# Kernel optimization log

Measured on AMD Instinct MI355X. Metric: run time of the kernel, lower is better.

The kernel has to match this reference:

```python
import jax, jax.numpy as jnp
import numpy as np

D_MODEL = 1024
H = 16
D_K = D_MODEL // H


def setup_inputs() -> dict:
    key = jax.random.key(0)
    ks = jax.random.split(key, 8)
    B, S = 2, 2048
    scale = 1.0 / np.sqrt(D_MODEL)
    return {
        "query": jax.random.normal(ks[0], (B, S, D_MODEL), dtype=jnp.float32),
        "key": jax.random.normal(ks[1], (B, S, D_MODEL), dtype=jnp.float32),
        "value": jax.random.normal(ks[2], (B, S, D_MODEL), dtype=jnp.float32),
        "mask": jnp.ones((B, 1, 1, S), dtype=jnp.int32),
        "Wq": jax.random.normal(ks[3], (D_MODEL, D_MODEL), dtype=jnp.float32) * scale,
        "Wk": jax.random.normal(ks[4], (D_MODEL, D_MODEL), dtype=jnp.float32) * scale,
        "Wv": jax.random.normal(ks[5], (D_MODEL, D_MODEL), dtype=jnp.float32) * scale,
        "Wo": jax.random.normal(ks[6], (D_MODEL, D_MODEL), dtype=jnp.float32) * scale,
    }


def reference(query, key, value, mask, Wq, Wk, Wv, Wo):
    # mask is a no-op in the original (masked_fill result discarded); dropout=0.
    B, S, _ = query.shape
    q = (query @ Wq.T).reshape(B, S, H, D_K)  # [B,S,H,Dk]
    k = (key @ Wk.T).reshape(B, S, H, D_K)
    v = (value @ Wv.T).reshape(B, S, H, D_K)
    # scores = Q K^T / sqrt(d_k)  -- NOTE: no softmax in the source module
    scores = jnp.einsum("bqhd,bkhd->bhqk", q, k) / jnp.sqrt(jnp.float32(D_K))
    out = jnp.einsum("bhqk,bkhd->bqhd", scores, v).reshape(B, S, D_MODEL)
    return out @ Wo.T
```

## Files before the change

### kernel.cpp

```cpp
#include <hip/hip_runtime.h>

#define DEV __device__ __forceinline__

typedef __attribute__((ext_vector_type(8))) short short8;
typedef __attribute__((ext_vector_type(4))) float f32x4;

DEV short f2bf(float x) {
  unsigned u = __float_as_uint(x);
  unsigned r = (u + 0x7fffu + ((u >> 16) & 1u)) >> 16;
  return (short)r;
}
DEV float bf2f(short x) {
  return __uint_as_float(((unsigned)(unsigned short)x) << 16);
}

DEV void gload_lds16(const void* g, void* l) {
  __builtin_amdgcn_global_load_lds((const __attribute__((address_space(1))) void*)g,
                                   (__attribute__((address_space(3))) void*)l, 16, 0, 0);
}

__global__ __launch_bounds__(256) void cvt_all(
    const float* __restrict__ s0, const float* __restrict__ s1,
    const float* __restrict__ s2, const float* __restrict__ s3,
    const float* __restrict__ s4, const float* __restrict__ s5,
    const float* __restrict__ s6,
    short* __restrict__ d0, short* __restrict__ d1, short* __restrict__ d2,
    short* __restrict__ d3, short* __restrict__ d4, short* __restrict__ d5,
    short* __restrict__ d6, float* __restrict__ Mb) {
  int g = blockIdx.x * 256 + threadIdx.x;
  if (g >= 2097152) {
    int off = g - 2097152;
    float4 z = {0.f, 0.f, 0.f, 0.f};
    float4* p = reinterpret_cast<float4*>(Mb) + (size_t)off * 2;
    p[0] = z;
    p[1] = z;
    return;
  }
  const float* s;
  short* d;
  int off;
  if (g < 524288) { s = s0; d = d0; off = g; }
  else if (g < 1048576) { s = s1; d = d1; off = g - 524288; }
  else if (g < 1572864) { s = s2; d = d2; off = g - 1048576; }
  else {
    int w2 = g - 1572864;
    int seg = w2 >> 17;
    off = w2 & 131071;
    s = seg == 0 ? s3 : seg == 1 ? s4 : seg == 2 ? s5 : s6;
    d = seg == 0 ? d3 : seg == 1 ? d4 : seg == 2 ? d5 : d6;
  }
  const float4* p = reinterpret_cast<const float4*>(s) + (size_t)off * 2;
  float4 a = p[0], b = p[1];
  short8 o;
  o[0] = f2bf(a.x); o[1] = f2bf(a.y); o[2] = f2bf(a.z); o[3] = f2bf(a.w);
  o[4] = f2bf(b.x); o[5] = f2bf(b.y); o[6] = f2bf(b.z); o[7] = f2bf(b.w);
  *reinterpret_cast<short8*>(d + (size_t)off * 8) = o;
}

template <typename OutT>
__global__ __launch_bounds__(256) void gemm_bt64(const short* __restrict__ A,
                                                 const short* __restrict__ W,
                                                 OutT* __restrict__ C,
                                                 long strideA, long strideW, long strideC) {
  __shared__ short At[128 * 64];
  __shared__ short Bt[64 * 64];
  const int nx = gridDim.x, ny = gridDim.y;
  int flat = blockIdx.x + nx * (blockIdx.y + ny * blockIdx.z);
  int nwg = nx * ny * gridDim.z;
  int l2 = (flat & 7) * (nwg >> 3) + (flat >> 3);
  int colB = l2 % nx;
  int tmp = l2 / nx;
  int rowB = tmp % ny;
  int zB = tmp / ny;

  const short* Ab = A + (size_t)zB * strideA;
  const short* Wb = W + (size_t)zB * strideW;
  OutT* Cb = C + (size_t)zB * strideC;
  const int t = threadIdx.x;
  const int w = t >> 6;
  const int l = t & 63;
  const int lg = l >> 4, lr = l & 15;
  const int wm = w >> 1, wn = w & 1;
  const int rowBase = rowB * 128;
  const int colBase = colB * 64;

  f32x4 acc[4][2] = {};

  for (int kt = 0; kt < 16; ++kt) {
    const int k0 = kt * 64;
    __syncthreads();
#pragma unroll
    for (int i = 0; i < 4; ++i) {
      int c = w * 256 + i * 64 + l;
      int r = c >> 3, s = c & 7;
      gload_lds16(Ab + (size_t)(rowBase + r) * 1024 + k0 + ((s ^ (r & 7)) << 3),
                  At + (size_t)c * 8);
    }
#pragma unroll
    for (int i = 0; i < 2; ++i) {
      int c = w * 128 + i * 64 + l;
      int r = c >> 3, s = c & 7;
      gload_lds16(Wb + (size_t)(colBase + r) * 1024 + k0 + ((s ^ (r & 7)) << 3),
                  Bt + (size_t)c * 8);
    }
    __syncthreads();
#pragma unroll
    for (int kk = 0; kk < 2; ++kk) {
      short8 bfr[2];
#pragma unroll
      for (int n = 0; n < 2; ++n) {
        int br = wn * 32 + n * 16 + lr;
        int slot = (kk * 4 + lg) ^ (br & 7);
        bfr[n] = *reinterpret_cast<const short8*>(&Bt[br * 64 + slot * 8]);
      }
#pragma unroll
      for (int m = 0; m < 4; ++m) {
        int ar = wm * 64 + m * 16 + lr;
        int slot = (kk * 4 + lg) ^ (ar & 7);
        short8 afr = *reinterpret_cast<const short8*>(&At[ar * 64 + slot * 8]);
        acc[m][0] = __builtin_amdgcn_mfma_f32_16x16x32_bf16(afr, bfr[0], acc[m][0], 0, 0, 0);
        acc[m][1] = __builtin_amdgcn_mfma_f32_16x16x32_bf16(afr, bfr[1], acc[m][1], 0, 0, 0);
      }
    }
  }
#pragma unroll
  for (int m = 0; m < 4; ++m)
#pragma unroll
    for (int n = 0; n < 2; ++n) {
      int row0 = rowBase + wm * 64 + m * 16 + lg * 4;
      int col = colBase + wn * 32 + n * 16 + lr;
#pragma unroll
      for (int j = 0; j < 4; ++j) {
        float v = acc[m][n][j];
        if constexpr (sizeof(OutT) == 2)
          Cb[(size_t)(row0 + j) * 1024 + col] = (OutT)f2bf(v);
        else
          Cb[(size_t)(row0 + j) * 1024 + col] = (OutT)v;
      }
    }
}

__global__ __launch_bounds__(256) void kv_outer(const short* __restrict__ Kp,
                                                const short* __restrict__ Vp,
                                                float* __restrict__ Mb) {
  __shared__ float Ks[128][64];
  __shared__ float Vs[128][64];
  const int t = threadIdx.x;
  const int sc = blockIdx.x, h = blockIdx.y, b = blockIdx.z;
  const size_t base = ((size_t)(b * 2048 + sc * 128)) * 1024 + h * 64;
  for (int e = t; e < 128 * 64; e += 256) {
    int r = e >> 6, c = e & 63;
    size_t g = base + (size_t)r * 1024 + c;
    Ks[r][c] = bf2f(Kp[g]);
    Vs[r][c] = bf2f(Vp[g]);
  }
  __syncthreads();
  const int dp0 = (t >> 4) * 4, d0 = (t & 15) * 4;
  float acc[4][4] = {};
  for (int s = 0; s < 128; ++s) {
    float4 kv = *reinterpret_cast<const float4*>(&Ks[s][dp0]);
    float4 vv = *reinterpret_cast<const float4*>(&Vs[s][d0]);
    float ka[4] = {kv.x, kv.y, kv.z, kv.w};
    float va[4] = {vv.x, vv.y, vv.z, vv.w};
#pragma unroll
    for (int i = 0; i < 4; ++i)
#pragma unroll
      for (int j = 0; j < 4; ++j) acc[i][j] += ka[i] * va[j];
  }
  float* dst = Mb + (size_t)(b * 16 + h) * 4096;
#pragma unroll
  for (int i = 0; i < 4; ++i)
#pragma unroll
    for (int j = 0; j < 4; ++j)
      atomicAdd(&dst[(dp0 + i) * 64 + d0 + j], acc[i][j] * 0.125f);
}

__global__ __launch_bounds__(256) void make_w2t(const float* __restrict__ Mb,
                                                const short* __restrict__ Wo,
                                                short* __restrict__ W2T) {
  __shared__ float Ms[64][65];
  __shared__ float Wos[64][64];
  const int t = threadIdx.x;
  const int jc = blockIdx.x, h = blockIdx.y, b = blockIdx.z;
  const float* Msrc = Mb + (size_t)(b * 16 + h) * 4096;
  for (int e = t; e < 4096; e += 256) {
    int r = e >> 6, c = e & 63;
    Ms[r][c] = Msrc[e];
    Wos[r][c] = bf2f(Wo[(size_t)(jc * 64 + r) * 1024 + h * 64 + c]);
  }
  __syncthreads();
  const int j0 = (t >> 4) * 4, p0 = (t & 15) * 4;
  float acc[4][4] = {};
  for (int d = 0; d < 64; ++d) {
    float wv[4], mv[4];
#pragma unroll
    for (int i = 0; i < 4; ++i) { wv[i] = Wos[j0 + i][d]; mv[i] = Ms[p0 + i][d]; }
#pragma unroll
    for (int i = 0; i < 4; ++i)
#pragma unroll
      for (int j2 = 0; j2 < 4; ++j2) acc[i][j2] += wv[i] * mv[j2];
  }
  short* dst = W2T + (size_t)b * 1048576;
#pragma unroll
  for (int i = 0; i < 4; ++i)
#pragma unroll
    for (int j2 = 0; j2 < 4; ++j2)
      dst[(size_t)(jc * 64 + j0 + i) * 1024 + h * 64 + p0 + j2] = f2bf(acc[i][j2]);
}

extern "C" void kernel_launch(void* const* d_in, const int* in_sizes, int n_in,
                              void* d_out, int out_size, void* d_ws, size_t ws_size,
                              hipStream_t stream) {
  const float* q  = (const float*)d_in[0];
  const float* k  = (const float*)d_in[1];
  const float* v  = (const float*)d_in[2];
  const float* Wq = (const float*)d_in[4];
  const float* Wk = (const float*)d_in[5];
  const float* Wv = (const float*)d_in[6];
  const float* Wo = (const float*)d_in[7];
  float* out = (float*)d_out;
  char* ws = (char*)d_ws;

  short* qkv = (short*)(ws);
  short* qb = qkv;
  short* kb = qkv + (size_t)4194304;
  short* vb = qkv + (size_t)8388608;
  short* wb = (short*)(ws + (24l << 20));
  short* wqb = wb;
  short* wkb = wb + 1048576;
  short* wvb = wb + 2097152;
  short* wob = wb + 3145728;
  short* Pp = (short*)(ws + (32l << 20));
  short* Qp = Pp;
  short* Kp = Pp + (size_t)4194304;
  short* Vp = Pp + (size_t)8388608;
  float* Mb  = (float*)(ws + (56l << 20));
  short* W2T = (short*)(ws + (57l << 20));

  cvt_all<<<8256, 256, 0, stream>>>(q, k, v, Wq, Wk, Wv, Wo,
                                    qb, kb, vb, wqb, wkb, wvb, wob, Mb);

  gemm_bt64<short><<<dim3(16, 32, 3), 256, 0, stream>>>(
      qkv, wb, Pp, 4194304l, 1048576l, 4194304l);

  kv_outer<<<dim3(16, 16, 2), 256, 0, stream>>>(Kp, Vp, Mb);

  make_w2t<<<dim3(16, 16, 2), 256, 0, stream>>>(Mb, wob, W2T);

  gemm_bt64<float><<<dim3(16, 16, 2), 256, 0, stream>>>(
      Qp, W2T, out, 2097152l, 1048576l, 2097152l);
}
```

Measured before the change: 209.1 us.

## Fuse fp32-to-bf16 conversion into QKV projection GEMM loads

Removes the separate conversion kernel and has the projection GEMM read fp32 inputs and weights directly, converting to bf16 in registers before writing swizzled LDS tiles. Global loads for the next k-tile are issued before the MFMA loop as register prefetch, and zeroing of the Mb accumulator moves into the first blocks. make_w2t now reads fp32 Wo directly. This drops a full kernel launch and the bf16 round trip through memory, but the GEMM reads twice as many bytes per tile, does its conversions inline, and no longer uses direct global-to-LDS loads.

```diff
diff --git a/kernel.cpp b/kernel.cpp
--- a/kernel.cpp
+++ b/kernel.cpp
@@ -19,42 +19,117 @@
                                    (__attribute__((address_space(3))) void*)l, 16, 0, 0);
 }
 
-__global__ __launch_bounds__(256) void cvt_all(
-    const float* __restrict__ s0, const float* __restrict__ s1,
-    const float* __restrict__ s2, const float* __restrict__ s3,
-    const float* __restrict__ s4, const float* __restrict__ s5,
-    const float* __restrict__ s6,
-    short* __restrict__ d0, short* __restrict__ d1, short* __restrict__ d2,
-    short* __restrict__ d3, short* __restrict__ d4, short* __restrict__ d5,
-    short* __restrict__ d6, float* __restrict__ Mb) {
-  int g = blockIdx.x * 256 + threadIdx.x;
-  if (g >= 2097152) {
-    int off = g - 2097152;
+__global__ __launch_bounds__(256) void gemm_proj_f32(
+    const float* __restrict__ q, const float* __restrict__ k, const float* __restrict__ v,
+    const float* __restrict__ Wq, const float* __restrict__ Wk, const float* __restrict__ Wv,
+    short* __restrict__ C, long strideC, float* __restrict__ Mb) {
+  __shared__ short At[128 * 64];
+  __shared__ short Bt[64 * 64];
+  const int t = threadIdx.x;
+  const int nx = gridDim.x, ny = gridDim.y;
+  int flat = blockIdx.x + nx * (blockIdx.y + ny * blockIdx.z);
+  int nwg = nx * ny * gridDim.z;
+  if (flat < 64) {
     float4 z = {0.f, 0.f, 0.f, 0.f};
-    float4* p = reinterpret_cast<float4*>(Mb) + (size_t)off * 2;
+    float4* p = reinterpret_cast<float4*>(Mb) + (size_t)flat * 512 + t * 2;
     p[0] = z;
     p[1] = z;
-    return;
-  }
-  const float* s;
-  short* d;
-  int off;
-  if (g < 524288) { s = s0; d = d0; off = g; }
-  else if (g < 1048576) { s = s1; d = d1; off = g - 524288; }
-  else if (g < 1572864) { s = s2; d = d2; off = g - 1048576; }
-  else {
-    int w2 = g - 1572864;
-    int seg = w2 >> 17;
-    off = w2 & 131071;
-    s = seg == 0 ? s3 : seg == 1 ? s4 : seg == 2 ? s5 : s6;
-    d = seg == 0 ? d3 : seg == 1 ? d4 : seg == 2 ? d5 : d6;
-  }
-  const float4* p = reinterpret_cast<const float4*>(s) + (size_t)off * 2;
-  float4 a = p[0], b = p[1];
-  short8 o;
-  o[0] = f2bf(a.x); o[1] = f2bf(a.y); o[2] = f2bf(a.z); o[3] = f2bf(a.w);
-  o[4] = f2bf(b.x); o[5] = f2bf(b.y); o[6] = f2bf(b.z); o[7] = f2bf(b.w);
-  *reinterpret_cast<short8*>(d + (size_t)off * 8) = o;
+  }
+  int l2 = (flat & 7) * (nwg >> 3) + (flat >> 3);
+  int colB = l2 % nx;
+  int tmp = l2 / nx;
+  int rowB = tmp % ny;
+  int zB = tmp / ny;
+
+  const float* Ab = zB == 0 ? q : zB == 1 ? k : v;
+  const float* Wb = zB == 0 ? Wq : zB == 1 ? Wk : Wv;
+  short* Cb = C + (size_t)zB * strideC;
+  const int w = t >> 6;
+  const int l = t & 63;
+  const int lg = l >> 4, lr = l & 15;
+  const int wm = w >> 1, wn = w & 1;
+  const int rowBase = rowB * 128;
+  const int colBase = colB * 64;
+
+  f32x4 acc[4][2] = {};
+  float4 ra[4][2], rw[2][2];
+
+#define LOAD_TILES(k0)                                                     \
+  {                                                                        \
+    _Pragma("unroll") for (int i = 0; i < 4; ++i) {                        \
+      int c = w * 256 + i * 64 + l;                                        \
+      int r = c >> 3, s = c & 7;                                           \
+      const float* src = Ab + (size_t)(rowBase + r) * 1024 + (k0) + s * 8; \
+      ra[i][0] = *reinterpret_cast<const float4*>(src);                    \
+      ra[i][1] = *reinterpret_cast<const float4*>(src + 4);                \
+    }                                                                      \
+    _Pragma("unroll") for (int i = 0; i < 2; ++i) {                        \
+      int c = w * 128 + i * 64 + l;                                        \
+      int r = c >> 3, s = c & 7;                                           \
+      const float* src = Wb + (size_t)(colBase + r) * 1024 + (k0) + s * 8; \
+      rw[i][0] = *reinterpret_cast<const float4*>(src);                    \
+      rw[i][1] = *reinterpret_cast<const float4*>(src + 4);                \
+    }                                                                      \
+  }
+
+  LOAD_TILES(0);
+
+  for (int kt = 0; kt < 16; ++kt) {
+    __syncthreads();
+#pragma unroll
+    for (int i = 0; i < 4; ++i) {
+      int c = w * 256 + i * 64 + l;
+      int r = c >> 3, s = c & 7;
+      short8 o;
+      o[0] = f2bf(ra[i][0].x); o[1] = f2bf(ra[i][0].y);
+      o[2] = f2bf(ra[i][0].z); o[3] = f2bf(ra[i][0].w);
+      o[4] = f2bf(ra[i][1].x); o[5] = f2bf(ra[i][1].y);
+      o[6] = f2bf(ra[i][1].z); o[7] = f2bf(ra[i][1].w);
+      *reinterpret_cast<short8*>(&At[r * 64 + ((s ^ (r & 7)) << 3)]) = o;
+    }
+#pragma unroll
+    for (int i = 0; i < 2; ++i) {
+      int c = w * 128 + i * 64 + l;
+      int r = c >> 3, s = c & 7;
+      short8 o;
+      o[0] = f2bf(rw[i][0].x); o[1] = f2bf(rw[i][0].y);
+      o[2] = f2bf(rw[i][0].z); o[3] = f2bf(rw[i][0].w);
+      o[4] = f2bf(rw[i][1].x); o[5] = f2bf(rw[i][1].y);
+      o[6] = f2bf(rw[i][1].z); o[7] = f2bf(rw[i][1].w);
+      *reinterpret_cast<short8*>(&Bt[r * 64 + ((s ^ (r & 7)) << 3)]) = o;
+    }
+    if (kt < 15) LOAD_TILES((kt + 1) * 64);
+    __syncthreads();
+#pragma unroll
+    for (int kk = 0; kk < 2; ++kk) {
+      short8 bfr[2];
+#pragma unroll
+      for (int n = 0; n < 2; ++n) {
+        int br = wn * 32 + n * 16 + lr;
+        int slot = (kk * 4 + lg) ^ (br & 7);
+        bfr[n] = *reinterpret_cast<const short8*>(&Bt[br * 64 + slot * 8]);
+      }
+#pragma unroll
+      for (int m = 0; m < 4; ++m) {
+        int ar = wm * 64 + m * 16 + lr;
+        int slot = (kk * 4 + lg) ^ (ar & 7);
+        short8 afr = *reinterpret_cast<const short8*>(&At[ar * 64 + slot * 8]);
+        acc[m][0] = __builtin_amdgcn_mfma_f32_16x16x32_bf16(afr, bfr[0], acc[m][0], 0, 0, 0);
+        acc[m][1] = __builtin_amdgcn_mfma_f32_16x16x32_bf16(afr, bfr[1], acc[m][1], 0, 0, 0);
+      }
+    }
+  }
+#undef LOAD_TILES
+#pragma unroll
+  for (int m = 0; m < 4; ++m)
+#pragma unroll
+    for (int n = 0; n < 2; ++n) {
+      int row0 = rowBase + wm * 64 + m * 16 + lg * 4;
+      int col = colBase + wn * 32 + n * 16 + lr;
+#pragma unroll
+      for (int j = 0; j < 4; ++j)
+        Cb[(size_t)(row0 + j) * 1024 + col] = f2bf(acc[m][n][j]);
+    }
 }
 
 template <typename OutT>
@@ -176,7 +251,7 @@
 }
 
 __global__ __launch_bounds__(256) void make_w2t(const float* __restrict__ Mb,
-                                                const short* __restrict__ Wo,
+                                                const float* __restrict__ Wo,
                                                 short* __restrict__ W2T) {
   __shared__ float Ms[64][65];
   __shared__ float Wos[64][64];
@@ -186,7 +261,7 @@
   for (int e = t; e < 4096; e += 256) {
     int r = e >> 6, c = e & 63;
     Ms[r][c] = Msrc[e];
-    Wos[r][c] = bf2f(Wo[(size_t)(jc * 64 + r) * 1024 + h * 64 + c]);
+    Wos[r][c] = Wo[(size_t)(jc * 64 + r) * 1024 + h * 64 + c];
   }
   __syncthreads();
   const int j0 = (t >> 4) * 4, p0 = (t & 15) * 4;
@@ -221,31 +296,19 @@
   float* out = (float*)d_out;
   char* ws = (char*)d_ws;
 
-  short* qkv = (short*)(ws);
-  short* qb = qkv;
-  short* kb = qkv + (size_t)4194304;
-  short* vb = qkv + (size_t)8388608;
-  short* wb = (short*)(ws + (24l << 20));
-  short* wqb = wb;
-  short* wkb = wb + 1048576;
-  short* wvb = wb + 2097152;
-  short* wob = wb + 3145728;
-  short* Pp = (short*)(ws + (32l << 20));
+  short* Pp = (short*)(ws);
   short* Qp = Pp;
   short* Kp = Pp + (size_t)4194304;
   short* Vp = Pp + (size_t)8388608;
-  float* Mb  = (float*)(ws + (56l << 20));
-  short* W2T = (short*)(ws + (57l << 20));
-
-  cvt_all<<<8256, 256, 0, stream>>>(q, k, v, Wq, Wk, Wv, Wo,
-                                    qb, kb, vb, wqb, wkb, wvb, wob, Mb);
-
-  gemm_bt64<short><<<dim3(16, 32, 3), 256, 0, stream>>>(
-      qkv, wb, Pp, 4194304l, 1048576l, 4194304l);
+  float* Mb  = (float*)(ws + (24l << 20));
+  short* W2T = (short*)(ws + (25l << 20));
+
+  gemm_proj_f32<<<dim3(16, 32, 3), 256, 0, stream>>>(
+      q, k, v, Wq, Wk, Wv, Pp, 4194304l, Mb);
 
   kv_outer<<<dim3(16, 16, 2), 256, 0, stream>>>(Kp, Vp, Mb);
 
-  make_w2t<<<dim3(16, 16, 2), 256, 0, stream>>>(Mb, wob, W2T);
+  make_w2t<<<dim3(16, 16, 2), 256, 0, stream>>>(Mb, Wo, W2T);
 
   gemm_bt64<float><<<dim3(16, 16, 2), 256, 0, stream>>>(
       Qp, W2T, out, 2097152l, 1048576l, 2097152l);
```

Result: slower. 227.1 us (+8.6%).
